# Optimization experiments

Hardware: AMD Instinct MI355X
Metric: run time of the kernel (lower is better)

## Reference

```python
import jax, jax.numpy as jnp
import numpy as np
from jax import lax


def _conv2d(x, w, b, pad):
    out = lax.conv_general_dilated(x, w, window_strides=(1, 1),
                                   padding=[(pad, pad), (pad, pad)])
    return out + b[None, :, None, None]


def _modulated_deform_conv(x, off_w, off_b, w, b, k, pad):
    """Modulated deformable conv (deformable_groups=1, stride=1, 'same' pad)."""
    B, C, H, W = x.shape
    K2 = k * k
    # offset/mask conv: 3*K2 channels -> (dy, dx, mask_logits)
    om = _conv2d(x, off_w, off_b, pad)              # [B, 3*K2, H, W]
    dy, dx, mlog = om[:, :K2], om[:, K2:2 * K2], om[:, 2 * K2:]
    mask = jax.nn.sigmoid(mlog)                     # [B, K2, H, W]

    xp = jnp.pad(x, ((0, 0), (0, 0), (pad, pad), (pad, pad)))
    Hp, Wp = H + 2 * pad, W + 2 * pad
    Ho, Wo = H, W                                   # stride 1, pad = k//2

    ky, kx = jnp.meshgrid(jnp.arange(k), jnp.arange(k), indexing='ij')
    ky = ky.reshape(1, K2, 1, 1).astype(x.dtype)
    kx = kx.reshape(1, K2, 1, 1).astype(x.dtype)
    iy = jnp.arange(Ho, dtype=x.dtype).reshape(1, 1, Ho, 1)
    ix = jnp.arange(Wo, dtype=x.dtype).reshape(1, 1, 1, Wo)

    py = iy + ky + dy                               # [B, K2, Ho, Wo] sample y (padded coords)
    px = ix + kx + dx                               # [B, K2, Ho, Wo] sample x

    y0f = jnp.floor(py); x0f = jnp.floor(px)
    ty = py - y0f; tx = px - x0f
    y0 = y0f.astype(jnp.int32); x0 = x0f.astype(jnp.int32)
    y1 = y0 + 1; x1 = x0 + 1

    xp_flat = xp.reshape(B, C, Hp * Wp)

    def gather(yi, xi):
        valid = ((yi >= 0) & (yi < Hp) & (xi >= 0) & (xi < Wp)).astype(x.dtype)
        yc = jnp.clip(yi, 0, Hp - 1)
        xc = jnp.clip(xi, 0, Wp - 1)
        idx = (yc * Wp + xc).reshape(B, 1, K2 * Ho * Wo)
        v = jnp.take_along_axis(xp_flat, idx, axis=2).reshape(B, C, K2, Ho, Wo)
        return v * valid[:, None]                   # zero-pad outside

    w00 = ((1 - ty) * (1 - tx))[:, None]
    w01 = ((1 - ty) * tx)[:, None]
    w10 = (ty * (1 - tx))[:, None]
    w11 = (ty * tx)[:, None]

    cols = (gather(y0, x0) * w00 + gather(y0, x1) * w01 +
            gather(y1, x0) * w10 + gather(y1, x1) * w11)
    cols = cols * mask[:, None]                     # [B, C, K2, Ho, Wo]

    O = w.shape[0]
    out = jnp.einsum('bckhw,ock->bohw', cols, w.reshape(O, C, K2))
    return out + b[None, :, None, None]


def setup_inputs() -> dict:
    key = jax.random.key(0)
    ks = jax.random.split(key, 12)
    B, Cin, H, W = 8, 64, 56, 56
    Ch = 128  # out_channels // 2

    def rn(k, shape, scale):
        return jax.random.normal(k, shape, dtype=jnp.float32) * scale

    return {
        'x': rn(ks[0], (B, Cin, H, W), 1.0),
        'w3': rn(ks[1], (Ch, Cin, 3, 3), 0.05),
        'b3': rn(ks[2], (Ch,), 0.05),
        'off3_w': rn(ks[3], (3 * 9, Cin, 3, 3), 0.01),
        'off3_b': rn(ks[4], (3 * 9,), 0.01),
        'w5': rn(ks[5], (Ch, Cin, 5, 5), 0.03),
        'b5': rn(ks[6], (Ch,), 0.05),
        'off5_w': rn(ks[7], (3 * 25, Cin, 5, 5), 0.01),
        'off5_b': rn(ks[8], (3 * 25,), 0.01),
        'sub_w': rn(ks[9], (Ch, Cin, 1, 1), 0.1),
        'sub_b': rn(ks[10], (Ch,), 0.05),
    }


def reference(x, w3, b3, off3_w, off3_b, w5, b5, off5_w, off5_b, sub_w, sub_b):
    x3 = _modulated_deform_conv(x, off3_w, off3_b, w3, b3, k=3, pad=1)
    x5 = _modulated_deform_conv(x, off5_w, off5_b, w5, b5, k=5, pad=2)
    xs = _conv2d(x, sub_w, sub_b, pad=0)            # 1x1 shortcut projection
    x3 = x3 + xs
    x5 = x5 + xs
    out = jnp.concatenate((x3, x5), axis=1)
    return jax.nn.relu(out)
```

## Files before the change

### kernel.cpp

```cpp
#include <hip/hip_runtime.h>
#include <hip/hip_bf16.h>
#include <math.h>

typedef __attribute__((ext_vector_type(8))) short short8;
typedef __attribute__((ext_vector_type(4))) float f32x4;

#define US_XP    0
#define N_XP     (8*60*60*64)
#define US_WOFF  (US_XP + N_XP)
#define N_WOFF   (26*2*8*64*8)
#define US_W5    (US_WOFF + N_WOFF)
#define N_W5     (26*2*8*64*8)
#define US_W3    (US_W5 + N_W5)
#define N_W3     (10*2*8*64*8)
#define US_TOT   (US_W3 + N_W3)
#define FB_BYTES (((US_TOT*2) + 15) & ~15)
#define F_BOM    0
#define F_B5     128
#define F_B3     256
#define N_ITEMS  (8*34*3136)
#define F_OFFS   384
#define F_WTS    (F_OFFS + N_ITEMS*4)

__device__ __forceinline__ unsigned short f2bf(float f) {
    union { float f; unsigned u; } v; v.f = f;
    unsigned r = v.u + 0x7FFFu + ((v.u >> 16) & 1u);
    return (unsigned short)(r >> 16);
}
__device__ __forceinline__ unsigned pack2(float lo, float hi) {
    __hip_bfloat162 h = __float22bfloat162_rn(make_float2(lo, hi));
    return *(unsigned*)&h;
}
__device__ __forceinline__ unsigned blend2(unsigned a, unsigned b, unsigned c, unsigned d,
                                           float w00, float w01, float w10, float w11) {
    float lo = __uint_as_float(a << 16) * w00 + __uint_as_float(b << 16) * w01
             + __uint_as_float(c << 16) * w10 + __uint_as_float(d << 16) * w11;
    float hi = __uint_as_float(a & 0xffff0000u) * w00 + __uint_as_float(b & 0xffff0000u) * w01
             + __uint_as_float(c & 0xffff0000u) * w10 + __uint_as_float(d & 0xffff0000u) * w11;
    return pack2(lo, hi);
}

__global__ __launch_bounds__(256) void prep_kernel(
    const float* __restrict__ x,
    const float* __restrict__ w3, const float* __restrict__ b3,
    const float* __restrict__ off3w, const float* __restrict__ off3b,
    const float* __restrict__ w5, const float* __restrict__ b5,
    const float* __restrict__ off5w, const float* __restrict__ off5b,
    const float* __restrict__ subw, const float* __restrict__ subb,
    unsigned short* __restrict__ us, float* __restrict__ fb)
{
    const int NTOT = US_TOT + 384;
    for (int i = blockIdx.x*256 + threadIdx.x; i < NTOT; i += gridDim.x*256) {
        if (i < US_TOT) {
            float v = 0.f;
            if (i < US_WOFF) {
                int c = i & 63, t = i >> 6;
                int xx = t % 60; t /= 60;
                int yy = t % 60; int b = t / 60;
                int y = yy - 2, xc = xx - 2;
                if ((unsigned)y < 56u && (unsigned)xc < 56u)
                    v = x[((b*64 + c)*56 + y)*56 + xc];
            } else {
                int j, mode;
                if (i < US_W5)      { j = i - US_WOFF; mode = 0; }
                else if (i < US_W3) { j = i - US_W5;   mode = 1; }
                else                { j = i - US_W3;   mode = 2; }
                int j8   = j & 7;
                int lane = (j >> 3) & 63;
                int oct  = (j >> 9) & 7;
                int kt   = (j >> 12) & 1;
                int tap  = j >> 13;
                int oc   = oct*16 + (lane & 15);
                int c    = kt*32 + (lane >> 4)*8 + j8;
                if (mode == 0) {
                    if (oc < 27 && tap < 25) {
                        int ky = tap/5, kx = tap%5;
                        if (ky>=1 && ky<=3 && kx>=1 && kx<=3)
                            v = off3w[((oc*64 + c)*3 + (ky-1))*3 + (kx-1)];
                    } else if (oc >= 27 && oc < 102 && tap < 25) {
                        v = off5w[((oc-27)*64 + c)*25 + tap];
                    }
                } else if (mode == 1) {
                    v = (tap < 25) ? w5[(oc*64 + c)*25 + tap] : subw[oc*64 + c];
                } else {
                    v = (tap < 9) ? w3[(oc*64 + c)*9 + tap] : subw[oc*64 + c];
                }
            }
            us[i] = f2bf(v);
        } else {
            int fj = i - US_TOT;
            float v;
            if (fj < 128)      v = (fj < 27) ? off3b[fj] : ((fj < 102) ? off5b[fj-27] : 0.f);
            else if (fj < 256) { int o = fj-128; v = b5[o] + subb[o]; }
            else               { int o = fj-256; v = b3[o] + subb[o]; }
            fb[fj] = v;
        }
    }
}

__global__ __launch_bounds__(256, 4) void convo2(
    const unsigned short* __restrict__ xp,
    const unsigned short* __restrict__ wp, const float* __restrict__ bias,
    int4* __restrict__ offs, uint2* __restrict__ wts)
{
    const int b    = blockIdx.y;
    const int pix0 = blockIdx.x * 64;
    const int lane = threadIdx.x & 63;
    const int wave = threadIdx.x >> 6;
    const int r15 = lane & 15, q4 = lane >> 4;
    const int cg  = lane & 7,  pr = lane >> 3;

    __shared__ __align__(16) unsigned short cols[2][2][64*72];

    f32x4 acc[2][4];
#pragma unroll
    for (int i = 0; i < 2; ++i)
#pragma unroll
        for (int pt = 0; pt < 4; ++pt) acc[i][pt] = (f32x4){0.f,0.f,0.f,0.f};

    const char* xb = (const char*)(xp + (size_t)b*(60*60*64));

    int coff[2];
#pragma unroll
    for (int it = 0; it < 2; ++it) {
        const int px  = wave*16 + it*8 + pr;
        const int pix = pix0 + px;
        const int oy  = pix/56, ox = pix - oy*56;
        coff[it] = (((oy+2)*60) + ox + 2) << 7;
    }

    auto stage_tap = [&](int t, unsigned short* buf) {
        int koff = 0;
        if (t < 25) { int ky = t/5, kx = t - ky*5; koff = ((ky-2)*60 + (kx-2)) << 7; }
#pragma unroll
        for (int it = 0; it < 2; ++it) {
            const int px = wave*16 + it*8 + pr;
            uint4 res = *(const uint4*)(xb + coff[it] + koff + cg*16);
            *(uint4*)&buf[px*72 + cg*8] = res;
        }
    };
    auto gemm_tap = [&](int tap, const unsigned short* buf) {
#pragma unroll
        for (int kt = 0; kt < 2; ++kt) {
            short8 Af[2];
#pragma unroll
            for (int i = 0; i < 2; ++i)
                Af[i] = *(const short8*)(wp + ((size_t)((tap*2+kt)*8 + wave*2 + i)*64 + lane)*8);
#pragma unroll
            for (int pt = 0; pt < 4; ++pt) {
                short8 Bf = *(const short8*)(buf + (pt*16 + r15)*72 + kt*32 + q4*8);
#pragma unroll
                for (int i = 0; i < 2; ++i)
                    acc[i][pt] = __builtin_amdgcn_mfma_f32_16x16x32_bf16(Af[i], Bf, acc[i][pt], 0, 0, 0);
            }
        }
    };

    stage_tap(0, cols[0][0]);
    stage_tap(1, cols[0][1]);
    __syncthreads();
    for (int r = 0; r < 13; ++r) {
        if (r + 1 < 13) {
            stage_tap(2*r+2, cols[(r+1)&1][0]);
            stage_tap(2*r+3, cols[(r+1)&1][1]);
        }
        gemm_tap(2*r,   cols[r&1][0]);
        gemm_tap(2*r+1, cols[r&1][1]);
        __syncthreads();
    }

    float* omt = (float*)cols;
#pragma unroll
    for (int i = 0; i < 2; ++i)
#pragma unroll
    for (int pt = 0; pt < 4; ++pt)
#pragma unroll
    for (int reg = 0; reg < 4; ++reg) {
        const int oc = (wave*2 + i)*16 + q4*4 + reg;
        const int px = pt*16 + r15;
        omt[oc*64 + px] = acc[i][pt][reg] + bias[oc];
    }
    __syncthreads();

    const int tid = threadIdx.x;
#pragma unroll
    for (int itr = 0; itr < 9; ++itr) {
        const int idx = itr*256 + tid;
        if (idx >= 34*64) break;
        const int t  = idx >> 6;
        const int px = idx & 63;
        const int pix = pix0 + px;
        const int oy = pix/56, ox = pix - oy*56;
        int ky, kx, cdy, cdx, cml, HP, SH;
        if (t < 25) { ky = t/5; kx = t%5; cdy = 27+t; cdx = 52+t; cml = 77+t; HP = 60; SH = 0; }
        else { int tt = t-25; ky = tt/3; kx = tt%3; cdy = tt; cdx = 9+tt; cml = 18+tt; HP = 58; SH = 1; }
        const float dy = omt[cdy*64 + px];
        const float dx = omt[cdx*64 + px];
        const float ml = omt[cml*64 + px];
        const float mask = 1.f / (1.f + __expf(-ml));
        const float py = (float)(oy + ky) + dy;
        const float qx = (float)(ox + kx) + dx;
        const float y0f = floorf(py), x0f = floorf(qx);
        const float ty = py - y0f, tx = qx - x0f;
        const int y0 = (int)y0f, x0 = (int)x0f, y1 = y0+1, x1 = x0+1;
        float w00 = (1.f-ty)*(1.f-tx)*mask;
        float w01 = (1.f-ty)*tx*mask;
        float w10 = ty*(1.f-tx)*mask;
        float w11 = ty*tx*mask;
        const bool vy0 = (unsigned)y0 < (unsigned)HP, vy1 = (unsigned)y1 < (unsigned)HP;
        const bool vx0 = (unsigned)x0 < (unsigned)HP, vx1 = (unsigned)x1 < (unsigned)HP;
        if (!(vy0 && vx0)) w00 = 0.f;
        if (!(vy0 && vx1)) w01 = 0.f;
        if (!(vy1 && vx0)) w10 = 0.f;
        if (!(vy1 && vx1)) w11 = 0.f;
        const int yc0 = min(max(y0,0),HP-1)+SH, yc1 = min(max(y1,0),HP-1)+SH;
        const int xc0 = min(max(x0,0),HP-1)+SH, xc1 = min(max(x1,0),HP-1)+SH;
        const int mi = (b*34 + t)*3136 + pix;
        offs[mi] = make_int4((yc0*60+xc0)<<7, (yc0*60+xc1)<<7, (yc1*60+xc0)<<7, (yc1*60+xc1)<<7);
        wts[mi]  = make_uint2(pack2(w00,w01), pack2(w10,w11));
    }
}

__global__ __launch_bounds__(256, 4) void convd2(
    const unsigned short* __restrict__ xp,
    const int4* __restrict__ offs, const uint2* __restrict__ wts,
    float* __restrict__ out,
    const unsigned short* __restrict__ wp5, const float* __restrict__ bias5,
    const unsigned short* __restrict__ wp3, const float* __restrict__ bias3)
{
    const int kind  = blockIdx.z;
    const unsigned short* wp = kind ? wp3 : wp5;
    const float* bias = kind ? bias3 : bias5;
    const int R     = kind ? 5  : 13;
    const int K2    = kind ? 9  : 25;
    const int tofs  = kind ? 25 : 0;
    const int outc0 = kind ? 0  : 128;

    const int b    = blockIdx.y;
    const int pix0 = blockIdx.x * 64;
    const int lane = threadIdx.x & 63;
    const int wave = threadIdx.x >> 6;
    const int r15 = lane & 15, q4 = lane >> 4;
    const int cg  = lane & 7,  pr = lane >> 3;

    __shared__ __align__(16) unsigned short cols[2][2][64*72];

    f32x4 acc[2][4];
#pragma unroll
    for (int i = 0; i < 2; ++i)
#pragma unroll
        for (int pt = 0; pt < 4; ++pt) acc[i][pt] = (f32x4){0.f,0.f,0.f,0.f};

    const char* xb = (const char*)(xp + (size_t)b*(60*60*64));

    int coff[2], mbase[2];
#pragma unroll
    for (int it = 0; it < 2; ++it) {
        const int px  = wave*16 + it*8 + pr;
        const int pix = pix0 + px;
        const int oy  = pix/56, ox = pix - oy*56;
        coff[it]  = (((oy+2)*60) + ox + 2) << 7;
        mbase[it] = (b*34 + tofs)*3136 + pix;
    }

    auto stage_tap = [&](int t, unsigned short* buf) {
#pragma unroll
        for (int it = 0; it < 2; ++it) {
            const int px = wave*16 + it*8 + pr;
            uint4 res;
            if (t >= K2) {
                res = *(const uint4*)(xb + coff[it] + cg*16);
            } else {
                const int mi = mbase[it] + t*3136;
                const int4 o4 = offs[mi];
                const uint2 wq = wts[mi];
                const float w00 = __uint_as_float(wq.x << 16);
                const float w01 = __uint_as_float(wq.x & 0xffff0000u);
                const float w10 = __uint_as_float(wq.y << 16);
                const float w11 = __uint_as_float(wq.y & 0xffff0000u);
                const uint4 qa = *(const uint4*)(xb + o4.x + cg*16);
                const uint4 qb = *(const uint4*)(xb + o4.y + cg*16);
                const uint4 qc = *(const uint4*)(xb + o4.z + cg*16);
                const uint4 qd = *(const uint4*)(xb + o4.w + cg*16);
                res.x = blend2(qa.x, qb.x, qc.x, qd.x, w00, w01, w10, w11);
                res.y = blend2(qa.y, qb.y, qc.y, qd.y, w00, w01, w10, w11);
                res.z = blend2(qa.z, qb.z, qc.z, qd.z, w00, w01, w10, w11);
                res.w = blend2(qa.w, qb.w, qc.w, qd.w, w00, w01, w10, w11);
            }
            *(uint4*)&buf[px*72 + cg*8] = res;
        }
    };
    auto gemm_tap = [&](int tap, const unsigned short* buf) {
#pragma unroll
        for (int kt = 0; kt < 2; ++kt) {
            short8 Af[2];
#pragma unroll
            for (int i = 0; i < 2; ++i)
                Af[i] = *(const short8*)(wp + ((size_t)((tap*2+kt)*8 + wave*2 + i)*64 + lane)*8);
#pragma unroll
            for (int pt = 0; pt < 4; ++pt) {
                short8 Bf = *(const short8*)(buf + (pt*16 + r15)*72 + kt*32 + q4*8);
#pragma unroll
                for (int i = 0; i < 2; ++i)
                    acc[i][pt] = __builtin_amdgcn_mfma_f32_16x16x32_bf16(Af[i], Bf, acc[i][pt], 0, 0, 0);
            }
        }
    };

    stage_tap(0, cols[0][0]);
    stage_tap(1, cols[0][1]);
    __syncthreads();
    for (int r = 0; r < R; ++r) {
        if (r + 1 < R) {
            stage_tap(2*r+2, cols[(r+1)&1][0]);
            stage_tap(2*r+3, cols[(r+1)&1][1]);
        }
        gemm_tap(2*r,   cols[r&1][0]);
        gemm_tap(2*r+1, cols[r&1][1]);
        __syncthreads();
    }

#pragma unroll
    for (int i = 0; i < 2; ++i)
#pragma unroll
    for (int pt = 0; pt < 4; ++pt)
#pragma unroll
    for (int reg = 0; reg < 4; ++reg) {
        const int oc  = (wave*2 + i)*16 + q4*4 + reg;
        const int pix = pix0 + pt*16 + r15;
        float v = fmaxf(acc[i][pt][reg] + bias[oc], 0.f);
        out[((size_t)b*256 + outc0 + oc)*3136 + pix] = v;
    }
}

extern "C" void kernel_launch(void* const* d_in, const int* in_sizes, int n_in,
                              void* d_out, int out_size, void* d_ws, size_t ws_size,
                              hipStream_t stream)
{
    (void)in_sizes; (void)n_in; (void)out_size; (void)ws_size;
    const float* x     = (const float*)d_in[0];
    const float* w3    = (const float*)d_in[1];
    const float* b3    = (const float*)d_in[2];
    const float* off3w = (const float*)d_in[3];
    const float* off3b = (const float*)d_in[4];
    const float* w5    = (const float*)d_in[5];
    const float* b5    = (const float*)d_in[6];
    const float* off5w = (const float*)d_in[7];
    const float* off5b = (const float*)d_in[8];
    const float* subw  = (const float*)d_in[9];
    const float* subb  = (const float*)d_in[10];

    unsigned short* us = (unsigned short*)d_ws;
    float* fb   = (float*)((char*)d_ws + FB_BYTES);
    int4*  offs = (int4*)(fb + F_OFFS);
    uint2* wts  = (uint2*)(fb + F_WTS);
    float* out  = (float*)d_out;

    prep_kernel<<<dim3(1024), dim3(256), 0, stream>>>(
        x, w3, b3, off3w, off3b, w5, b5, off5w, off5b, subw, subb, us, fb);

    convo2<<<dim3(49, 8), dim3(256), 0, stream>>>(
        us + US_XP, us + US_WOFF, fb + F_BOM, offs, wts);

    convd2<<<dim3(49, 8, 2), dim3(256), 0, stream>>>(
        us + US_XP, offs, wts, out,
        us + US_W5, fb + F_B5, us + US_W3, fb + F_B3);
}
```

Measured before the change: 173.5 us.

## Halve pixel tile and software-pipeline global loads across MFMA in conv kernels

Both conv kernels now work on 32-pixel tiles instead of 64, doubling the grid so more blocks can spread across compute units, and they raise the launch-bounds occupancy hints. Staging is split into an issue phase that puts global loads into registers before the MFMA work and a commit phase that blends and writes to LDS afterwards, so memory latency overlaps compute. The deformable kernel also prefetches offset/weight metadata one round ahead. This costs more registers per thread and reloads the weight fragments once per smaller tile.

```diff
diff --git a/kernel.cpp b/kernel.cpp
--- a/kernel.cpp
+++ b/kernel.cpp
@@ -98,74 +98,63 @@
     }
 }
 
-__global__ __launch_bounds__(256, 4) void convo2(
+__global__ __launch_bounds__(256, 6) void convo3(
     const unsigned short* __restrict__ xp,
     const unsigned short* __restrict__ wp, const float* __restrict__ bias,
     int4* __restrict__ offs, uint2* __restrict__ wts)
 {
     const int b    = blockIdx.y;
-    const int pix0 = blockIdx.x * 64;
+    const int pix0 = blockIdx.x * 32;
     const int lane = threadIdx.x & 63;
     const int wave = threadIdx.x >> 6;
     const int r15 = lane & 15, q4 = lane >> 4;
     const int cg  = lane & 7,  pr = lane >> 3;
 
-    __shared__ __align__(16) unsigned short cols[2][2][64*72];
-
-    f32x4 acc[2][4];
-#pragma unroll
-    for (int i = 0; i < 2; ++i)
-#pragma unroll
-        for (int pt = 0; pt < 4; ++pt) acc[i][pt] = (f32x4){0.f,0.f,0.f,0.f};
+    __shared__ __align__(16) unsigned short cols[2][2][32*72];
+
+    f32x4 acc[2][2] = {{{0.f,0.f,0.f,0.f},{0.f,0.f,0.f,0.f}},
+                       {{0.f,0.f,0.f,0.f},{0.f,0.f,0.f,0.f}}};
 
     const char* xb = (const char*)(xp + (size_t)b*(60*60*64));
-
-    int coff[2];
-#pragma unroll
-    for (int it = 0; it < 2; ++it) {
-        const int px  = wave*16 + it*8 + pr;
-        const int pix = pix0 + px;
-        const int oy  = pix/56, ox = pix - oy*56;
-        coff[it] = (((oy+2)*60) + ox + 2) << 7;
-    }
-
-    auto stage_tap = [&](int t, unsigned short* buf) {
-        int koff = 0;
-        if (t < 25) { int ky = t/5, kx = t - ky*5; koff = ((ky-2)*60 + (kx-2)) << 7; }
-#pragma unroll
-        for (int it = 0; it < 2; ++it) {
-            const int px = wave*16 + it*8 + pr;
-            uint4 res = *(const uint4*)(xb + coff[it] + koff + cg*16);
-            *(uint4*)&buf[px*72 + cg*8] = res;
-        }
-    };
-    auto gemm_tap = [&](int tap, const unsigned short* buf) {
+    const int px  = wave*8 + pr;
+    const int pix = pix0 + px;
+    const int oy  = pix/56, ox = pix - oy*56;
+    const int coff = (((oy+2)*60) + ox + 2) << 7;
+
+    uint4 G0, G1;
+    auto issue = [&](int ta, int tb) {
+        int ka = 0, kb = 0;
+        if (ta < 25) { int ky = ta/5, kx = ta - ky*5; ka = ((ky-2)*60 + (kx-2)) << 7; }
+        if (tb < 25) { int ky = tb/5, kx = tb - ky*5; kb = ((ky-2)*60 + (kx-2)) << 7; }
+        G0 = *(const uint4*)(xb + coff + ka + cg*16);
+        G1 = *(const uint4*)(xb + coff + kb + cg*16);
+    };
+    auto commit = [&](unsigned short* bufa, unsigned short* bufb) {
+        *(uint4*)&bufa[px*72 + cg*8] = G0;
+        *(uint4*)&bufb[px*72 + cg*8] = G1;
+    };
+    auto gemm = [&](int tap, const unsigned short* buf) {
 #pragma unroll
         for (int kt = 0; kt < 2; ++kt) {
-            short8 Af[2];
-#pragma unroll
-            for (int i = 0; i < 2; ++i)
-                Af[i] = *(const short8*)(wp + ((size_t)((tap*2+kt)*8 + wave*2 + i)*64 + lane)*8);
-#pragma unroll
-            for (int pt = 0; pt < 4; ++pt) {
+            short8 A0 = *(const short8*)(wp + ((size_t)((tap*2+kt)*8 + wave*2    )*64 + lane)*8);
+            short8 A1 = *(const short8*)(wp + ((size_t)((tap*2+kt)*8 + wave*2 + 1)*64 + lane)*8);
+#pragma unroll
+            for (int pt = 0; pt < 2; ++pt) {
                 short8 Bf = *(const short8*)(buf + (pt*16 + r15)*72 + kt*32 + q4*8);
-#pragma unroll
-                for (int i = 0; i < 2; ++i)
-                    acc[i][pt] = __builtin_amdgcn_mfma_f32_16x16x32_bf16(Af[i], Bf, acc[i][pt], 0, 0, 0);
+                acc[0][pt] = __builtin_amdgcn_mfma_f32_16x16x32_bf16(A0, Bf, acc[0][pt], 0, 0, 0);
+                acc[1][pt] = __builtin_amdgcn_mfma_f32_16x16x32_bf16(A1, Bf, acc[1][pt], 0, 0, 0);
             }
         }
     };
 
-    stage_tap(0, cols[0][0]);
-    stage_tap(1, cols[0][1]);
+    issue(0, 1);
+    commit(cols[0][0], cols[0][1]);
     __syncthreads();
     for (int r = 0; r < 13; ++r) {
-        if (r + 1 < 13) {
-            stage_tap(2*r+2, cols[(r+1)&1][0]);
-            stage_tap(2*r+3, cols[(r+1)&1][1]);
-        }
-        gemm_tap(2*r,   cols[r&1][0]);
-        gemm_tap(2*r+1, cols[r&1][1]);
+        if (r + 1 < 13) issue(2*r+2, 2*r+3);
+        gemm(2*r,   cols[r&1][0]);
+        gemm(2*r+1, cols[r&1][1]);
+        if (r + 1 < 13) commit(cols[(r+1)&1][0], cols[(r+1)&1][1]);
         __syncthreads();
     }
 
@@ -173,33 +162,33 @@
 #pragma unroll
     for (int i = 0; i < 2; ++i)
 #pragma unroll
-    for (int pt = 0; pt < 4; ++pt)
+    for (int pt = 0; pt < 2; ++pt)
 #pragma unroll
     for (int reg = 0; reg < 4; ++reg) {
         const int oc = (wave*2 + i)*16 + q4*4 + reg;
-        const int px = pt*16 + r15;
-        omt[oc*64 + px] = acc[i][pt][reg] + bias[oc];
+        const int p2 = pt*16 + r15;
+        omt[oc*32 + p2] = acc[i][pt][reg] + bias[oc];
     }
     __syncthreads();
 
     const int tid = threadIdx.x;
 #pragma unroll
-    for (int itr = 0; itr < 9; ++itr) {
+    for (int itr = 0; itr < 5; ++itr) {
         const int idx = itr*256 + tid;
-        if (idx >= 34*64) break;
-        const int t  = idx >> 6;
-        const int px = idx & 63;
-        const int pix = pix0 + px;
-        const int oy = pix/56, ox = pix - oy*56;
+        if (idx >= 34*32) break;
+        const int t  = idx >> 5;
+        const int p2 = idx & 31;
+        const int pix2 = pix0 + p2;
+        const int oy2 = pix2/56, ox2 = pix2 - oy2*56;
         int ky, kx, cdy, cdx, cml, HP, SH;
         if (t < 25) { ky = t/5; kx = t%5; cdy = 27+t; cdx = 52+t; cml = 77+t; HP = 60; SH = 0; }
         else { int tt = t-25; ky = tt/3; kx = tt%3; cdy = tt; cdx = 9+tt; cml = 18+tt; HP = 58; SH = 1; }
-        const float dy = omt[cdy*64 + px];
-        const float dx = omt[cdx*64 + px];
-        const float ml = omt[cml*64 + px];
+        const float dy = omt[cdy*32 + p2];
+        const float dx = omt[cdx*32 + p2];
+        const float ml = omt[cml*32 + p2];
         const float mask = 1.f / (1.f + __expf(-ml));
-        const float py = (float)(oy + ky) + dy;
-        const float qx = (float)(ox + kx) + dx;
+        const float py = (float)(oy2 + ky) + dy;
+        const float qx = (float)(ox2 + kx) + dx;
         const float y0f = floorf(py), x0f = floorf(qx);
         const float ty = py - y0f, tx = qx - x0f;
         const int y0 = (int)y0f, x0 = (int)x0f, y1 = y0+1, x1 = x0+1;
@@ -215,13 +204,13 @@
         if (!(vy1 && vx1)) w11 = 0.f;
         const int yc0 = min(max(y0,0),HP-1)+SH, yc1 = min(max(y1,0),HP-1)+SH;
         const int xc0 = min(max(x0,0),HP-1)+SH, xc1 = min(max(x1,0),HP-1)+SH;
-        const int mi = (b*34 + t)*3136 + pix;
+        const int mi = (b*34 + t)*3136 + pix2;
         offs[mi] = make_int4((yc0*60+xc0)<<7, (yc0*60+xc1)<<7, (yc1*60+xc0)<<7, (yc1*60+xc1)<<7);
         wts[mi]  = make_uint2(pack2(w00,w01), pack2(w10,w11));
     }
 }
 
-__global__ __launch_bounds__(256, 4) void convd2(
+__global__ __launch_bounds__(256, 5) void convd3(
     const unsigned short* __restrict__ xp,
     const int4* __restrict__ offs, const uint2* __restrict__ wts,
     float* __restrict__ out,
@@ -237,99 +226,126 @@
     const int outc0 = kind ? 0  : 128;
 
     const int b    = blockIdx.y;
-    const int pix0 = blockIdx.x * 64;
+    const int pix0 = blockIdx.x * 32;
     const int lane = threadIdx.x & 63;
     const int wave = threadIdx.x >> 6;
     const int r15 = lane & 15, q4 = lane >> 4;
     const int cg  = lane & 7,  pr = lane >> 3;
 
-    __shared__ __align__(16) unsigned short cols[2][2][64*72];
-
-    f32x4 acc[2][4];
-#pragma unroll
-    for (int i = 0; i < 2; ++i)
-#pragma unroll
-        for (int pt = 0; pt < 4; ++pt) acc[i][pt] = (f32x4){0.f,0.f,0.f,0.f};
+    __shared__ __align__(16) unsigned short cols[2][2][32*72];
+
+    f32x4 acc[2][2] = {{{0.f,0.f,0.f,0.f},{0.f,0.f,0.f,0.f}},
+                       {{0.f,0.f,0.f,0.f},{0.f,0.f,0.f,0.f}}};
 
     const char* xb = (const char*)(xp + (size_t)b*(60*60*64));
-
-    int coff[2], mbase[2];
-#pragma unroll
-    for (int it = 0; it < 2; ++it) {
-        const int px  = wave*16 + it*8 + pr;
-        const int pix = pix0 + px;
-        const int oy  = pix/56, ox = pix - oy*56;
-        coff[it]  = (((oy+2)*60) + ox + 2) << 7;
-        mbase[it] = (b*34 + tofs)*3136 + pix;
-    }
-
-    auto stage_tap = [&](int t, unsigned short* buf) {
-#pragma unroll
-        for (int it = 0; it < 2; ++it) {
-            const int px = wave*16 + it*8 + pr;
-            uint4 res;
-            if (t >= K2) {
-                res = *(const uint4*)(xb + coff[it] + cg*16);
-            } else {
-                const int mi = mbase[it] + t*3136;
-                const int4 o4 = offs[mi];
-                const uint2 wq = wts[mi];
-                const float w00 = __uint_as_float(wq.x << 16);
-                const float w01 = __uint_as_float(wq.x & 0xffff0000u);
-                const float w10 = __uint_as_float(wq.y << 16);
-                const float w11 = __uint_as_float(wq.y & 0xffff0000u);
-                const uint4 qa = *(const uint4*)(xb + o4.x + cg*16);
-                const uint4 qb = *(const uint4*)(xb + o4.y + cg*16);
-                const uint4 qc = *(const uint4*)(xb + o4.z + cg*16);
-                const uint4 qd = *(const uint4*)(xb + o4.w + cg*16);
-                res.x = blend2(qa.x, qb.x, qc.x, qd.x, w00, w01, w10, w11);
-                res.y = blend2(qa.y, qb.y, qc.y, qd.y, w00, w01, w10, w11);
-                res.z = blend2(qa.z, qb.z, qc.z, qd.z, w00, w01, w10, w11);
-                res.w = blend2(qa.w, qb.w, qc.w, qd.w, w00, w01, w10, w11);
+    const int px  = wave*8 + pr;
+    const int pix = pix0 + px;
+    const int oy  = pix/56, ox = pix - oy*56;
+    const int coff  = (((oy+2)*60) + ox + 2) << 7;
+    const int mbase = (b*34 + tofs)*3136 + pix;
+
+    uint4 C0[4], C1[4];
+    uint2 WC0, WC1;
+    int4  MO0, MO1;
+    uint2 MW0, MW1;
+
+    auto load_meta = [&](int ta, int tb) {
+        const int a  = min(ta, K2-1) * 3136;
+        const int bb = min(tb, K2-1) * 3136;
+        MO0 = offs[mbase + a];  MW0 = wts[mbase + a];
+        MO1 = offs[mbase + bb]; MW1 = wts[mbase + bb];
+    };
+    auto issue = [&](int ta, int tb) {
+        if (ta >= K2) {
+            C0[0] = *(const uint4*)(xb + coff + cg*16);
+        } else {
+            WC0 = MW0;
+            C0[0] = *(const uint4*)(xb + MO0.x + cg*16);
+            C0[1] = *(const uint4*)(xb + MO0.y + cg*16);
+            C0[2] = *(const uint4*)(xb + MO0.z + cg*16);
+            C0[3] = *(const uint4*)(xb + MO0.w + cg*16);
+        }
+        if (tb >= K2) {
+            C1[0] = *(const uint4*)(xb + coff + cg*16);
+        } else {
+            WC1 = MW1;
+            C1[0] = *(const uint4*)(xb + MO1.x + cg*16);
+            C1[1] = *(const uint4*)(xb + MO1.y + cg*16);
+            C1[2] = *(const uint4*)(xb + MO1.z + cg*16);
+            C1[3] = *(const uint4*)(xb + MO1.w + cg*16);
+        }
+    };
+    auto commit = [&](int ta, int tb, unsigned short* bufa, unsigned short* bufb) {
+        uint4 res;
+        if (ta >= K2) {
+            res = C0[0];
+        } else {
+            const float w00 = __uint_as_float(WC0.x << 16);
+            const float w01 = __uint_as_float(WC0.x & 0xffff0000u);
+            const float w10 = __uint_as_float(WC0.y << 16);
+            const float w11 = __uint_as_float(WC0.y & 0xffff0000u);
+            res.x = blend2(C0[0].x, C0[1].x, C0[2].x, C0[3].x, w00, w01, w10, w11);
+            res.y = blend2(C0[0].y, C0[1].y, C0[2].y, C0[3].y, w00, w01, w10, w11);
+            res.z = blend2(C0[0].z, C0[1].z, C0[2].z, C0[3].z, w00, w01, w10, w11);
+            res.w = blend2(C0[0].w, C0[1].w, C0[2].w, C0[3].w, w00, w01, w10, w11);
+        }
+        *(uint4*)&bufa[px*72 + cg*8] = res;
+        if (tb >= K2) {
+            res = C1[0];
+        } else {
+            const float w00 = __uint_as_float(WC1.x << 16);
+            const float w01 = __uint_as_float(WC1.x & 0xffff0000u);
+            const float w10 = __uint_as_float(WC1.y << 16);
+            const float w11 = __uint_as_float(WC1.y & 0xffff0000u);
+            res.x = blend2(C1[0].x, C1[1].x, C1[2].x, C1[3].x, w00, w01, w10, w11);
+            res.y = blend2(C1[0].y, C1[1].y, C1[2].y, C1[3].y, w00, w01, w10, w11);
+            res.z = blend2(C1[0].z, C1[1].z, C1[2].z, C1[3].z, w00, w01, w10, w11);
+            res.w = blend2(C1[0].w, C1[1].w, C1[2].w, C1[3].w, w00, w01, w10, w11);
+        }
+        *(uint4*)&bufb[px*72 + cg*8] = res;
+    };
+    auto gemm = [&](int tap, const unsigned short* buf) {
+#pragma unroll
+        for (int kt = 0; kt < 2; ++kt) {
+            short8 A0 = *(const short8*)(wp + ((size_t)((tap*2+kt)*8 + wave*2    )*64 + lane)*8);
+            short8 A1 = *(const short8*)(wp + ((size_t)((tap*2+kt)*8 + wave*2 + 1)*64 + lane)*8);
+#pragma unroll
+            for (int pt = 0; pt < 2; ++pt) {
+                short8 Bf = *(const short8*)(buf + (pt*16 + r15)*72 + kt*32 + q4*8);
+                acc[0][pt] = __builtin_amdgcn_mfma_f32_16x16x32_bf16(A0, Bf, acc[0][pt], 0, 0, 0);
+                acc[1][pt] = __builtin_amdgcn_mfma_f32_16x16x32_bf16(A1, Bf, acc[1][pt], 0, 0, 0);
             }
-            *(uint4*)&buf[px*72 + cg*8] = res;
-        }
-    };
-    auto gemm_tap = [&](int tap, const unsigned short* buf) {
-#pragma unroll
-        for (int kt = 0; kt < 2; ++kt) {
-            short8 Af[2];
-#pragma unroll
-            for (int i = 0; i < 2; ++i)
-                Af[i] = *(const short8*)(wp + ((size_t)((tap*2+kt)*8 + wave*2 + i)*64 + lane)*8);
-#pragma unroll
-            for (int pt = 0; pt < 4; ++pt) {
-                short8 Bf = *(const short8*)(buf + (pt*16 + r15)*72 + kt*32 + q4*8);
-#pragma unroll
-                for (int i = 0; i < 2; ++i)
-                    acc[i][pt] = __builtin_amdgcn_mfma_f32_16x16x32_bf16(Af[i], Bf, acc[i][pt], 0, 0, 0);
-            }
-        }
-    };
-
-    stage_tap(0, cols[0][0]);
-    stage_tap(1, cols[0][1]);
+        }
+    };
+
+    load_meta(0, 1);
+    issue(0, 1);
+    load_meta(2, 3);
+    commit(0, 1, cols[0][0], cols[0][1]);
     __syncthreads();
+
     for (int r = 0; r < R; ++r) {
         if (r + 1 < R) {
-            stage_tap(2*r+2, cols[(r+1)&1][0]);
-            stage_tap(2*r+3, cols[(r+1)&1][1]);
-        }
-        gemm_tap(2*r,   cols[r&1][0]);
-        gemm_tap(2*r+1, cols[r&1][1]);
+            issue(2*r+2, 2*r+3);
+            load_meta(2*r+4, 2*r+5);
+        }
+        gemm(2*r,   cols[r&1][0]);
+        gemm(2*r+1, cols[r&1][1]);
+        if (r + 1 < R)
+            commit(2*r+2, 2*r+3, cols[(r+1)&1][0], cols[(r+1)&1][1]);
         __syncthreads();
     }
 
 #pragma unroll
     for (int i = 0; i < 2; ++i)
 #pragma unroll
-    for (int pt = 0; pt < 4; ++pt)
+    for (int pt = 0; pt < 2; ++pt)
 #pragma unroll
     for (int reg = 0; reg < 4; ++reg) {
         const int oc  = (wave*2 + i)*16 + q4*4 + reg;
-        const int pix = pix0 + pt*16 + r15;
+        const int p2  = pix0 + pt*16 + r15;
         float v = fmaxf(acc[i][pt][reg] + bias[oc], 0.f);
-        out[((size_t)b*256 + outc0 + oc)*3136 + pix] = v;
+        out[((size_t)b*256 + outc0 + oc)*3136 + p2] = v;
     }
 }
 
@@ -359,10 +375,10 @@
     prep_kernel<<<dim3(1024), dim3(256), 0, stream>>>(
         x, w3, b3, off3w, off3b, w5, b5, off5w, off5b, subw, subb, us, fb);
 
-    convo2<<<dim3(49, 8), dim3(256), 0, stream>>>(
+    convo3<<<dim3(98, 8), dim3(256), 0, stream>>>(
         us + US_XP, us + US_WOFF, fb + F_BOM, offs, wts);
 
-    convd2<<<dim3(49, 8, 2), dim3(256), 0, stream>>>(
+    convd3<<<dim3(98, 8, 2), dim3(256), 0, stream>>>(
         us + US_XP, offs, wts, out,
         us + US_W5, fb + F_B5, us + US_W3, fb + F_B3);
 }
```

Result: faster. 159.7 us (-8.0%).

## Load MFMA B fragments directly from global, dropping LDS staging and barriers

Applied to the files above, without the earlier changes.

Both the offset conv and the deformable conv now build their MFMA B operands straight from global memory in registers, so the LDS column buffers and per-round barriers are gone. The offset conv uses 32-pixel blocks, doubling its grid, and keeps LDS only for the epilogue. The deform conv gives each wave 4 output-channel tiles by 2 pixel tiles and prefetches the next tap's offsets and weights in registers. This cuts LDS traffic and synchronisation, but adds register pressure (launch bounds lowered to 3) and loses the cross-wave sharing of staged columns.

```diff
diff --git a/kernel.cpp b/kernel.cpp
--- a/kernel.cpp
+++ b/kernel.cpp
@@ -98,108 +98,78 @@
     }
 }
 
-__global__ __launch_bounds__(256, 4) void convo2(
+__global__ __launch_bounds__(256, 4) void convo4(
     const unsigned short* __restrict__ xp,
     const unsigned short* __restrict__ wp, const float* __restrict__ bias,
     int4* __restrict__ offs, uint2* __restrict__ wts)
 {
     const int b    = blockIdx.y;
-    const int pix0 = blockIdx.x * 64;
+    const int pix0 = blockIdx.x * 32;
     const int lane = threadIdx.x & 63;
     const int wave = threadIdx.x >> 6;
     const int r15 = lane & 15, q4 = lane >> 4;
-    const int cg  = lane & 7,  pr = lane >> 3;
-
-    __shared__ __align__(16) unsigned short cols[2][2][64*72];
-
-    f32x4 acc[2][4];
+
+    __shared__ float omt[128*33];
+
+    f32x4 acc[2][2] = {{{0.f,0.f,0.f,0.f},{0.f,0.f,0.f,0.f}},
+                       {{0.f,0.f,0.f,0.f},{0.f,0.f,0.f,0.f}}};
+
+    const char* xb = (const char*)(xp + (size_t)b*(60*60*64));
+    int bofs[2];
+#pragma unroll
+    for (int pt = 0; pt < 2; ++pt) {
+        const int pix = pix0 + pt*16 + r15;
+        const int oy = pix/56, ox = pix - oy*56;
+        bofs[pt] = ((oy+2)*60 + ox + 2)*128 + q4*16;
+    }
+
+#pragma unroll 5
+    for (int t = 0; t < 25; ++t) {
+        const int ky = t/5, kx = t - ky*5;
+        const int koff = ((ky-2)*60 + (kx-2))*128;
+#pragma unroll
+        for (int kt = 0; kt < 2; ++kt) {
+            short8 B0 = *(const short8*)(xb + bofs[0] + koff + kt*64);
+            short8 B1 = *(const short8*)(xb + bofs[1] + koff + kt*64);
+            short8 A0 = *(const short8*)(wp + ((size_t)((t*2+kt)*8 + wave*2    )*64 + lane)*8);
+            short8 A1 = *(const short8*)(wp + ((size_t)((t*2+kt)*8 + wave*2 + 1)*64 + lane)*8);
+            acc[0][0] = __builtin_amdgcn_mfma_f32_16x16x32_bf16(A0, B0, acc[0][0], 0, 0, 0);
+            acc[0][1] = __builtin_amdgcn_mfma_f32_16x16x32_bf16(A0, B1, acc[0][1], 0, 0, 0);
+            acc[1][0] = __builtin_amdgcn_mfma_f32_16x16x32_bf16(A1, B0, acc[1][0], 0, 0, 0);
+            acc[1][1] = __builtin_amdgcn_mfma_f32_16x16x32_bf16(A1, B1, acc[1][1], 0, 0, 0);
+        }
+    }
+
 #pragma unroll
     for (int i = 0; i < 2; ++i)
 #pragma unroll
-        for (int pt = 0; pt < 4; ++pt) acc[i][pt] = (f32x4){0.f,0.f,0.f,0.f};
-
-    const char* xb = (const char*)(xp + (size_t)b*(60*60*64));
-
-    int coff[2];
-#pragma unroll
-    for (int it = 0; it < 2; ++it) {
-        const int px  = wave*16 + it*8 + pr;
-        const int pix = pix0 + px;
-        const int oy  = pix/56, ox = pix - oy*56;
-        coff[it] = (((oy+2)*60) + ox + 2) << 7;
-    }
-
-    auto stage_tap = [&](int t, unsigned short* buf) {
-        int koff = 0;
-        if (t < 25) { int ky = t/5, kx = t - ky*5; koff = ((ky-2)*60 + (kx-2)) << 7; }
-#pragma unroll
-        for (int it = 0; it < 2; ++it) {
-            const int px = wave*16 + it*8 + pr;
-            uint4 res = *(const uint4*)(xb + coff[it] + koff + cg*16);
-            *(uint4*)&buf[px*72 + cg*8] = res;
-        }
-    };
-    auto gemm_tap = [&](int tap, const unsigned short* buf) {
-#pragma unroll
-        for (int kt = 0; kt < 2; ++kt) {
-            short8 Af[2];
-#pragma unroll
-            for (int i = 0; i < 2; ++i)
-                Af[i] = *(const short8*)(wp + ((size_t)((tap*2+kt)*8 + wave*2 + i)*64 + lane)*8);
-#pragma unroll
-            for (int pt = 0; pt < 4; ++pt) {
-                short8 Bf = *(const short8*)(buf + (pt*16 + r15)*72 + kt*32 + q4*8);
-#pragma unroll
-                for (int i = 0; i < 2; ++i)
-                    acc[i][pt] = __builtin_amdgcn_mfma_f32_16x16x32_bf16(Af[i], Bf, acc[i][pt], 0, 0, 0);
-            }
-        }
-    };
-
-    stage_tap(0, cols[0][0]);
-    stage_tap(1, cols[0][1]);
-    __syncthreads();
-    for (int r = 0; r < 13; ++r) {
-        if (r + 1 < 13) {
-            stage_tap(2*r+2, cols[(r+1)&1][0]);
-            stage_tap(2*r+3, cols[(r+1)&1][1]);
-        }
-        gemm_tap(2*r,   cols[r&1][0]);
-        gemm_tap(2*r+1, cols[r&1][1]);
-        __syncthreads();
-    }
-
-    float* omt = (float*)cols;
-#pragma unroll
-    for (int i = 0; i < 2; ++i)
-#pragma unroll
-    for (int pt = 0; pt < 4; ++pt)
+    for (int pt = 0; pt < 2; ++pt)
 #pragma unroll
     for (int reg = 0; reg < 4; ++reg) {
         const int oc = (wave*2 + i)*16 + q4*4 + reg;
-        const int px = pt*16 + r15;
-        omt[oc*64 + px] = acc[i][pt][reg] + bias[oc];
+        const int p2 = pt*16 + r15;
+        omt[oc*33 + p2] = acc[i][pt][reg] + bias[oc];
     }
     __syncthreads();
 
     const int tid = threadIdx.x;
 #pragma unroll
-    for (int itr = 0; itr < 9; ++itr) {
+    for (int itr = 0; itr < 5; ++itr) {
         const int idx = itr*256 + tid;
-        if (idx >= 34*64) break;
-        const int t  = idx >> 6;
-        const int px = idx & 63;
-        const int pix = pix0 + px;
-        const int oy = pix/56, ox = pix - oy*56;
+        if (idx >= 34*32) break;
+        const int t  = idx >> 5;
+        const int p2 = idx & 31;
+        const int pix2 = pix0 + p2;
+        const int oy2 = pix2/56, ox2 = pix2 - oy2*56;
         int ky, kx, cdy, cdx, cml, HP, SH;
         if (t < 25) { ky = t/5; kx = t%5; cdy = 27+t; cdx = 52+t; cml = 77+t; HP = 60; SH = 0; }
         else { int tt = t-25; ky = tt/3; kx = tt%3; cdy = tt; cdx = 9+tt; cml = 18+tt; HP = 58; SH = 1; }
-        const float dy = omt[cdy*64 + px];
-        const float dx = omt[cdx*64 + px];
-        const float ml = omt[cml*64 + px];
+        const float dy = omt[cdy*33 + p2];
+        const float dx = omt[cdx*33 + p2];
+        const float ml = omt[cml*33 + p2];
         const float mask = 1.f / (1.f + __expf(-ml));
-        const float py = (float)(oy + ky) + dy;
-        const float qx = (float)(ox + kx) + dx;
+        const float py = (float)(oy2 + ky) + dy;
+        const float qx = (float)(ox2 + kx) + dx;
         const float y0f = floorf(py), x0f = floorf(qx);
         const float ty = py - y0f, tx = qx - x0f;
         const int y0 = (int)y0f, x0 = (int)x0f, y1 = y0+1, x1 = x0+1;
@@ -215,118 +185,117 @@
         if (!(vy1 && vx1)) w11 = 0.f;
         const int yc0 = min(max(y0,0),HP-1)+SH, yc1 = min(max(y1,0),HP-1)+SH;
         const int xc0 = min(max(x0,0),HP-1)+SH, xc1 = min(max(x1,0),HP-1)+SH;
-        const int mi = (b*34 + t)*3136 + pix;
+        const int mi = (b*34 + t)*3136 + pix2;
         offs[mi] = make_int4((yc0*60+xc0)<<7, (yc0*60+xc1)<<7, (yc1*60+xc0)<<7, (yc1*60+xc1)<<7);
         wts[mi]  = make_uint2(pack2(w00,w01), pack2(w10,w11));
     }
 }
 
-__global__ __launch_bounds__(256, 4) void convd2(
+__global__ __launch_bounds__(256, 3) void convd4(
     const unsigned short* __restrict__ xp,
     const int4* __restrict__ offs, const uint2* __restrict__ wts,
     float* __restrict__ out,
     const unsigned short* __restrict__ wp5, const float* __restrict__ bias5,
     const unsigned short* __restrict__ wp3, const float* __restrict__ bias3)
 {
-    const int kind  = blockIdx.z;
+    const int kind = blockIdx.z;
     const unsigned short* wp = kind ? wp3 : wp5;
     const float* bias = kind ? bias3 : bias5;
-    const int R     = kind ? 5  : 13;
+    const int ntaps = kind ? 10 : 26;
     const int K2    = kind ? 9  : 25;
     const int tofs  = kind ? 25 : 0;
     const int outc0 = kind ? 0  : 128;
 
     const int b    = blockIdx.y;
-    const int pix0 = blockIdx.x * 64;
     const int lane = threadIdx.x & 63;
     const int wave = threadIdx.x >> 6;
     const int r15 = lane & 15, q4 = lane >> 4;
-    const int cg  = lane & 7,  pr = lane >> 3;
-
-    __shared__ __align__(16) unsigned short cols[2][2][64*72];
-
-    f32x4 acc[2][4];
-#pragma unroll
-    for (int i = 0; i < 2; ++i)
-#pragma unroll
-        for (int pt = 0; pt < 4; ++pt) acc[i][pt] = (f32x4){0.f,0.f,0.f,0.f};
+    const int ocq  = (wave & 1)*4;
+    const int pix0 = blockIdx.x*64 + (wave >> 1)*32;
+
+    f32x4 acc[4][2];
+#pragma unroll
+    for (int i = 0; i < 4; ++i)
+#pragma unroll
+        for (int pt = 0; pt < 2; ++pt) acc[i][pt] = (f32x4){0.f,0.f,0.f,0.f};
 
     const char* xb = (const char*)(xp + (size_t)b*(60*60*64));
 
-    int coff[2], mbase[2];
-#pragma unroll
-    for (int it = 0; it < 2; ++it) {
-        const int px  = wave*16 + it*8 + pr;
-        const int pix = pix0 + px;
-        const int oy  = pix/56, ox = pix - oy*56;
-        coff[it]  = (((oy+2)*60) + ox + 2) << 7;
-        mbase[it] = (b*34 + tofs)*3136 + pix;
-    }
-
-    auto stage_tap = [&](int t, unsigned short* buf) {
-#pragma unroll
-        for (int it = 0; it < 2; ++it) {
-            const int px = wave*16 + it*8 + pr;
-            uint4 res;
-            if (t >= K2) {
-                res = *(const uint4*)(xb + coff[it] + cg*16);
-            } else {
-                const int mi = mbase[it] + t*3136;
-                const int4 o4 = offs[mi];
-                const uint2 wq = wts[mi];
-                const float w00 = __uint_as_float(wq.x << 16);
-                const float w01 = __uint_as_float(wq.x & 0xffff0000u);
-                const float w10 = __uint_as_float(wq.y << 16);
-                const float w11 = __uint_as_float(wq.y & 0xffff0000u);
-                const uint4 qa = *(const uint4*)(xb + o4.x + cg*16);
-                const uint4 qb = *(const uint4*)(xb + o4.y + cg*16);
-                const uint4 qc = *(const uint4*)(xb + o4.z + cg*16);
-                const uint4 qd = *(const uint4*)(xb + o4.w + cg*16);
-                res.x = blend2(qa.x, qb.x, qc.x, qd.x, w00, w01, w10, w11);
-                res.y = blend2(qa.y, qb.y, qc.y, qd.y, w00, w01, w10, w11);
-                res.z = blend2(qa.z, qb.z, qc.z, qd.z, w00, w01, w10, w11);
-                res.w = blend2(qa.w, qb.w, qc.w, qd.w, w00, w01, w10, w11);
+    int coff[2], mb[2];
+#pragma unroll
+    for (int pt = 0; pt < 2; ++pt) {
+        const int pix = pix0 + pt*16 + r15;
+        const int oy = pix/56, ox = pix - oy*56;
+        coff[pt] = ((oy+2)*60 + ox + 2)*128 + q4*16;
+        mb[pt]   = (b*34 + tofs)*3136 + pix;
+    }
+
+    int4  MOn[2]; uint2 MWn[2];
+#pragma unroll
+    for (int pt = 0; pt < 2; ++pt) { MOn[pt] = offs[mb[pt]]; MWn[pt] = wts[mb[pt]]; }
+
+#pragma unroll 2
+    for (int t = 0; t < ntaps; ++t) {
+        int4 MOc[2]; uint2 MWc[2];
+#pragma unroll
+        for (int pt = 0; pt < 2; ++pt) { MOc[pt] = MOn[pt]; MWc[pt] = MWn[pt]; }
+        const int tn = min(t + 1, K2 - 1) * 3136;
+#pragma unroll
+        for (int pt = 0; pt < 2; ++pt) { MOn[pt] = offs[mb[pt] + tn]; MWn[pt] = wts[mb[pt] + tn]; }
+
+        short8 B[2][2];
+        if (t >= K2) {
+#pragma unroll
+            for (int kt = 0; kt < 2; ++kt)
+#pragma unroll
+                for (int pt = 0; pt < 2; ++pt)
+                    B[kt][pt] = *(const short8*)(xb + coff[pt] + kt*64);
+        } else {
+            uint4 c[2][2][4];
+#pragma unroll
+            for (int kt = 0; kt < 2; ++kt)
+#pragma unroll
+                for (int pt = 0; pt < 2; ++pt) {
+                    const int eo = kt*64 + q4*16;
+                    c[kt][pt][0] = *(const uint4*)(xb + MOc[pt].x + eo);
+                    c[kt][pt][1] = *(const uint4*)(xb + MOc[pt].y + eo);
+                    c[kt][pt][2] = *(const uint4*)(xb + MOc[pt].z + eo);
+                    c[kt][pt][3] = *(const uint4*)(xb + MOc[pt].w + eo);
+                }
+#pragma unroll
+            for (int kt = 0; kt < 2; ++kt)
+#pragma unroll
+                for (int pt = 0; pt < 2; ++pt) {
+                    const float w00 = __uint_as_float(MWc[pt].x << 16);
+                    const float w01 = __uint_as_float(MWc[pt].x & 0xffff0000u);
+                    const float w10 = __uint_as_float(MWc[pt].y << 16);
+                    const float w11 = __uint_as_float(MWc[pt].y & 0xffff0000u);
+                    uint4 r;
+                    r.x = blend2(c[kt][pt][0].x, c[kt][pt][1].x, c[kt][pt][2].x, c[kt][pt][3].x, w00, w01, w10, w11);
+                    r.y = blend2(c[kt][pt][0].y, c[kt][pt][1].y, c[kt][pt][2].y, c[kt][pt][3].y, w00, w01, w10, w11);
+                    r.z = blend2(c[kt][pt][0].z, c[kt][pt][1].z, c[kt][pt][2].z, c[kt][pt][3].z, w00, w01, w10, w11);
+                    r.w = blend2(c[kt][pt][0].w, c[kt][pt][1].w, c[kt][pt][2].w, c[kt][pt][3].w, w00, w01, w10, w11);
+                    B[kt][pt] = *(short8*)&r;
+                }
+        }
+#pragma unroll
+        for (int kt = 0; kt < 2; ++kt)
+#pragma unroll
+            for (int i = 0; i < 4; ++i) {
+                short8 A = *(const short8*)(wp + ((size_t)((t*2+kt)*8 + ocq + i)*64 + lane)*8);
+#pragma unroll
+                for (int pt = 0; pt < 2; ++pt)
+                    acc[i][pt] = __builtin_amdgcn_mfma_f32_16x16x32_bf16(A, B[kt][pt], acc[i][pt], 0, 0, 0);
             }
-            *(uint4*)&buf[px*72 + cg*8] = res;
-        }
-    };
-    auto gemm_tap = [&](int tap, const unsigned short* buf) {
-#pragma unroll
-        for (int kt = 0; kt < 2; ++kt) {
-            short8 Af[2];
-#pragma unroll
-            for (int i = 0; i < 2; ++i)
-                Af[i] = *(const short8*)(wp + ((size_t)((tap*2+kt)*8 + wave*2 + i)*64 + lane)*8);
-#pragma unroll
-            for (int pt = 0; pt < 4; ++pt) {
-                short8 Bf = *(const short8*)(buf + (pt*16 + r15)*72 + kt*32 + q4*8);
-#pragma unroll
-                for (int i = 0; i < 2; ++i)
-                    acc[i][pt] = __builtin_amdgcn_mfma_f32_16x16x32_bf16(Af[i], Bf, acc[i][pt], 0, 0, 0);
-            }
-        }
-    };
-
-    stage_tap(0, cols[0][0]);
-    stage_tap(1, cols[0][1]);
-    __syncthreads();
-    for (int r = 0; r < R; ++r) {
-        if (r + 1 < R) {
-            stage_tap(2*r+2, cols[(r+1)&1][0]);
-            stage_tap(2*r+3, cols[(r+1)&1][1]);
-        }
-        gemm_tap(2*r,   cols[r&1][0]);
-        gemm_tap(2*r+1, cols[r&1][1]);
-        __syncthreads();
-    }
-
-#pragma unroll
-    for (int i = 0; i < 2; ++i)
-#pragma unroll
-    for (int pt = 0; pt < 4; ++pt)
+    }
+
+#pragma unroll
+    for (int i = 0; i < 4; ++i)
+#pragma unroll
+    for (int pt = 0; pt < 2; ++pt)
 #pragma unroll
     for (int reg = 0; reg < 4; ++reg) {
-        const int oc  = (wave*2 + i)*16 + q4*4 + reg;
+        const int oc  = (ocq + i)*16 + q4*4 + reg;
         const int pix = pix0 + pt*16 + r15;
         float v = fmaxf(acc[i][pt][reg] + bias[oc], 0.f);
         out[((size_t)b*256 + outc0 + oc)*3136 + pix] = v;
@@ -359,10 +328,10 @@
     prep_kernel<<<dim3(1024), dim3(256), 0, stream>>>(
         x, w3, b3, off3w, off3b, w5, b5, off5w, off5b, subw, subb, us, fb);
 
-    convo2<<<dim3(49, 8), dim3(256), 0, stream>>>(
+    convo4<<<dim3(98, 8), dim3(256), 0, stream>>>(
         us + US_XP, us + US_WOFF, fb + F_BOM, offs, wts);
 
-    convd2<<<dim3(49, 8, 2), dim3(256), 0, stream>>>(
+    convd4<<<dim3(49, 8, 2), dim3(256), 0, stream>>>(
         us + US_XP, offs, wts, out,
         us + US_W5, fb + F_B5, us + US_W3, fb + F_B3);
 }
```

Result: slower. 275.1 us (+58.5%).
